# Kernel tuning notes

Measured on AMD Instinct MI355X. Metric: run time of the kernel, lower is better.

## Reference

```python
import jax, jax.numpy as jnp
import numpy as np

HEAD_SIZE = 64
BLOCK_SIZE = 4096
BATCH = 4


def setup_inputs() -> dict:
    key = jax.random.key(0)
    kx, kk, kq, kv = jax.random.split(key, 4)
    x = jax.random.normal(kx, (BATCH, BLOCK_SIZE, HEAD_SIZE), dtype=jnp.float32)
    s = HEAD_SIZE ** -0.5  # ~ torch default linear init scale
    Wk = jax.random.uniform(kk, (HEAD_SIZE, HEAD_SIZE), jnp.float32, -s, s)
    Wq = jax.random.uniform(kq, (HEAD_SIZE, HEAD_SIZE), jnp.float32, -s, s)
    Wv = jax.random.uniform(kv, (HEAD_SIZE, HEAD_SIZE), jnp.float32, -s, s)
    return {"x": x, "Wk": Wk, "Wq": Wq, "Wv": Wv}


def reference(x, Wk, Wq, Wv):
    # x: [B, T, C]; W*: [C, C] stored torch-style (out, in) -> y = x @ W.T
    B, T, C = x.shape
    k = x @ Wk.T  # [B, T, C]
    q = x @ Wq.T
    v = x @ Wv.T
    scores = jnp.einsum('btc,bsc->bts', q, k) * (C ** -0.5)  # [B, T, T]
    causal = jnp.tril(jnp.ones((T, T), dtype=bool))
    scores = jnp.where(causal, scores, -jnp.inf)
    weights = jax.nn.softmax(scores, axis=-1)
    out = jnp.einsum('bts,bsc->btc', weights, v)  # [B, T, C]
    return out
```

## Files before the change

kernel.cpp:

```cpp
#include <hip/hip_runtime.h>
#include <hip/hip_bf16.h>

typedef unsigned short u16;
typedef unsigned int u32;
typedef __bf16 bf16x8_t __attribute__((ext_vector_type(8)));
typedef float f32x4_t __attribute__((ext_vector_type(4)));

constexpr int Bb = 4;
constexpr int Tt = 4096;
constexpr int Dd = 64;
constexpr float QSCALE = 0.18033688011112042f;

__device__ __forceinline__ u16 f2bf(float f) {
  unsigned int u = __builtin_bit_cast(unsigned int, f);
  return (u16)((u + 0x7fffu + ((u >> 16) & 1u)) >> 16);
}
__device__ __forceinline__ u32 pk2(float a, float b) {
  return (u32)f2bf(a) | ((u32)f2bf(b) << 16);
}
__device__ __forceinline__ u32 pkt(float a, float b) {
  const u32 ua = __builtin_bit_cast(u32, a);
  const u32 ub = __builtin_bit_cast(u32, b);
  return (ua >> 16) | (ub & 0xFFFF0000u);
}
__device__ __forceinline__ bf16x8_t ld16(const u16* p) {
  int4 v = *(const int4*)p;
  return __builtin_bit_cast(bf16x8_t, v);
}
__device__ __forceinline__ f32x4_t mfma16(bf16x8_t a, bf16x8_t b, f32x4_t c) {
  return __builtin_amdgcn_mfma_f32_16x16x32_bf16(a, b, c, 0, 0, 0);
}

__global__ __launch_bounds__(256) void HeadV1_proj(
    const float* __restrict__ x, const float* __restrict__ Wk,
    const float* __restrict__ Wq, const float* __restrict__ Wv,
    u16* __restrict__ qS, u16* __restrict__ kS, u16* __restrict__ vS)
{
  __shared__ u16 xl[64][72];
  __shared__ u16 Wl[3][64][72];
  __shared__ u16 ylds[64][72];

  const int t = threadIdx.x;
  const int w = t >> 6, lane = t & 63, l15 = lane & 15, quad = lane >> 4;
  const int r0 = blockIdx.x * 64;
  const int b  = r0 >> 12;
  const int kt = (r0 & 4095) >> 6;
  const long tilebase = ((long)(b * 64 + kt)) * 4096;

  {
    const float* srcs[4] = {x + (long)r0 * 64, Wk, Wq, Wv};
    u16* dstl[4] = {&xl[0][0], &Wl[0][0][0], &Wl[1][0][0], &Wl[2][0][0]};
    #pragma unroll
    for (int mm = 0; mm < 4; mm++) {
      const float* s = srcs[mm];
      u16* d = dstl[mm];
      #pragma unroll
      for (int i = 0; i < 4; i++) {
        const int f4 = i * 256 + t;
        const int row = f4 >> 4, c4 = f4 & 15;
        float4 v = ((const float4*)(s + row * 64))[c4];
        uint2 pk;
        pk.x = pk2(v.x, v.y);
        pk.y = pk2(v.z, v.w);
        *(uint2*)(d + row * 72 + c4 * 4) = pk;
      }
    }
  }
  __syncthreads();

  bf16x8_t xf[2];
  #pragma unroll
  for (int kh = 0; kh < 2; kh++)
    xf[kh] = ld16(&xl[w * 16 + l15][kh * 32 + quad * 8]);

  u16* dsts[3];
  dsts[0] = kS + tilebase; dsts[1] = qS + tilebase; dsts[2] = vS + tilebase;

  #pragma unroll
  for (int m = 0; m < 3; m++) {
    float vals[4][4];
    #pragma unroll
    for (int g = 0; g < 4; g++) {
      f32x4_t acc = {0.f, 0.f, 0.f, 0.f};
      #pragma unroll
      for (int kh = 0; kh < 2; kh++) {
        bf16x8_t wf = ld16(&Wl[m][g * 16 + l15][kh * 32 + quad * 8]);
        acc = mfma16(xf[kh], wf, acc);
      }
      #pragma unroll
      for (int r = 0; r < 4; r++)
        vals[g][r] = (m == 1) ? acc[r] * QSCALE : acc[r];
    }
    #pragma unroll
    for (int g = 0; g < 4; g++)
      #pragma unroll
      for (int r = 0; r < 4; r++)
        ylds[w * 16 + quad * 4 + r][g * 16 + l15] = f2bf(vals[g][r]);
    __syncthreads();
    if (m < 2) {
      #pragma unroll
      for (int kk = 0; kk < 2; kk++) {
        bf16x8_t f = ld16(&ylds[w * 16 + l15][kk * 32 + quad * 8]);
        *(int4*)(dsts[m] + (w * 2 + kk) * 512 + lane * 8) = __builtin_bit_cast(int4, f);
      }
    } else {
      #pragma unroll
      for (int kk = 0; kk < 2; kk++) {
        u16 tmp[8];
        #pragma unroll
        for (int j = 0; j < 8; j++)
          tmp[j] = ylds[kk * 32 + quad * 8 + j][w * 16 + l15];
        *(int4*)(dsts[2] + (kk * 4 + w) * 512 + lane * 8) = *(const int4*)tmp;
      }
    }
    __syncthreads();
  }
}

__global__ __launch_bounds__(1024, 4) void HeadV1_flash(
    const u16* __restrict__ qS, const u16* __restrict__ kS,
    const u16* __restrict__ vS, float* __restrict__ outg)
{
  __shared__ __align__(16) char smem[53248];
  u16  (*pT)[32][36]   = (u16 (*)[32][36])smem;
  float (*chk)[16][33] = (float (*)[16][33])smem;
  float (*stg)[32][68] = (float (*)[32][68])(smem + 33792);
  float (*lst)[32]     = (float (*)[32])(smem + 33792 + 17408);

  const int t    = threadIdx.x;
  const int w    = t >> 6;
  const int lane = t & 63;
  const int l15  = lane & 15;
  const int quad = lane >> 4;

  const int b  = blockIdx.x & 3;
  const int i  = blockIdx.x >> 2;
  const int j1 = i, j2 = 127 - i;
  const int nk1 = (j1 >> 1) + 1;
  const int nk2 = (j2 >> 1) + 1;
  int n1 = (16 * nk1 + 32) / 65;
  if (n1 < 1) n1 = 1;
  if (n1 > 15) n1 = 15;

  const bool grp2 = (w >= n1);
  const int j   = grp2 ? j2 : j1;
  const int nk  = grp2 ? nk2 : nk1;
  const int str = grp2 ? (16 - n1) : n1;
  const int off = grp2 ? (w - n1) : w;

  const int qt64 = j >> 1;
  const int ql0  = (j & 1) * 32;
  const int qr0  = j * 32;
  const long base = (long)b * Tt * Dd;

  union { u32 u4[4]; bf16x8_t v; } uo;
  uo.u4[0] = uo.u4[1] = uo.u4[2] = uo.u4[3] = 0x3F803F80u;
  const bf16x8_t ones = uo.v;
  const f32x4_t zero4 = {0.f, 0.f, 0.f, 0.f};

  const u16* qtile = qS + ((long)(b * 64 + qt64)) * 4096 + lane * 8;
  bf16x8_t qfrag[2][2];
  #pragma unroll
  for (int ct = 0; ct < 2; ct++)
    #pragma unroll
    for (int kd = 0; kd < 2; kd++)
      qfrag[ct][kd] = ld16(qtile + ((ql0 / 16 + ct) * 2 + kd) * 512);

  f32x4_t O[4][2];
  #pragma unroll
  for (int a = 0; a < 4; a++)
    #pragma unroll
    for (int c = 0; c < 2; c++)
      O[a][c] = zero4;
  f32x4_t Lc[2] = {zero4, zero4};

  for (int kt = off; kt < nk; kt += str) {
    const bool ismask = (kt == nk - 1);
    const int kv0 = kt * 64;
    const u16* ktile = kS + ((long)(b * 64 + kt)) * 4096 + lane * 8;
    const u16* vtile = vS + ((long)(b * 64 + kt)) * 4096 + lane * 8;

    #pragma unroll
    for (int kk = 0; kk < 2; kk++) {
      bf16x8_t vf[4];
      #pragma unroll
      for (int dt = 0; dt < 4; dt++)
        vf[dt] = ld16(vtile + (kk * 4 + dt) * 512);

      #pragma unroll
      for (int rtl = 0; rtl < 2; rtl++) {
        const int rt = kk * 2 + rtl;
        bf16x8_t kf0 = ld16(ktile + (rt * 2 + 0) * 512);
        bf16x8_t kf1 = ld16(ktile + (rt * 2 + 1) * 512);
        #pragma unroll
        for (int ct = 0; ct < 2; ct++) {
          f32x4_t acc = zero4;
          acc = mfma16(kf0, qfrag[ct][0], acc);
          acc = mfma16(kf1, qfrag[ct][1], acc);
          if (ismask) {
            const int kvl = kv0 + rt * 16 + quad * 4;
            const int qi  = qr0 + ct * 16 + l15;
            #pragma unroll
            for (int r = 0; r < 4; r++)
              if (kvl + r > qi) acc[r] = -1e30f;
          }
          const float p0 = __builtin_amdgcn_exp2f(acc[0]);
          const float p1 = __builtin_amdgcn_exp2f(acc[1]);
          const float p2 = __builtin_amdgcn_exp2f(acc[2]);
          const float p3 = __builtin_amdgcn_exp2f(acc[3]);
          uint2 pk;
          pk.x = pkt(p0, p1);
          pk.y = pkt(p2, p3);
          *(uint2*)&pT[w][ct * 16 + l15][rtl * 16 + quad * 4] = pk;
        }
      }
      #pragma unroll
      for (int ct = 0; ct < 2; ct++) {
        bf16x8_t pf = ld16(&pT[w][ct * 16 + l15][quad * 8]);
        #pragma unroll
        for (int dt = 0; dt < 4; dt++)
          O[dt][ct] = mfma16(vf[dt], pf, O[dt][ct]);
        Lc[ct] = mfma16(ones, pf, Lc[ct]);
      }
    }
  }

  if (quad == 0) {
    #pragma unroll
    for (int ct = 0; ct < 2; ct++)
      lst[w][ct * 16 + l15] = Lc[ct][0];
  }
  __syncthreads();

  #pragma unroll
  for (int dt = 0; dt < 4; dt++) {
    #pragma unroll
    for (int ct = 0; ct < 2; ct++)
      #pragma unroll
      for (int r = 0; r < 4; r++)
        chk[w][quad * 4 + r][ct * 16 + l15] = O[dt][ct][r];
    __syncthreads();
    {
      const int jsel = t >> 9, tt = t & 511;
      const int d2 = tt >> 5, q = tt & 31;
      const int lo = jsel ? n1 : 0, hi = jsel ? 16 : n1;
      float s = 0.f;
      for (int w2 = lo; w2 < hi; w2++) s += chk[w2][d2][q];
      stg[jsel][q][dt * 16 + d2] = s;
    }
    __syncthreads();
  }

  {
    const int jsel = t >> 9, tt = t & 511;
    const int q = tt >> 4, dg = tt & 15;
    const int lo = jsel ? n1 : 0, hi = jsel ? 16 : n1;
    float L = 0.f;
    for (int w2 = lo; w2 < hi; w2++) L += lst[w2][q];
    const float invL = 1.0f / L;
    const int jj = jsel ? j2 : j1;
    float4 v = *(const float4*)&stg[jsel][q][dg * 4];
    v.x *= invL; v.y *= invL; v.z *= invL; v.w *= invL;
    *(float4*)(outg + base + (long)(jj * 32 + q) * 64 + dg * 4) = v;
  }
}

extern "C" void kernel_launch(void* const* d_in, const int* in_sizes, int n_in,
                              void* d_out, int out_size, void* d_ws, size_t ws_size,
                              hipStream_t stream) {
  (void)in_sizes; (void)n_in; (void)out_size; (void)ws_size;
  const float* x  = (const float*)d_in[0];
  const float* Wk = (const float*)d_in[1];
  const float* Wq = (const float*)d_in[2];
  const float* Wv = (const float*)d_in[3];
  float* out = (float*)d_out;
  u16* qw  = (u16*)d_ws;
  u16* kw  = qw + (size_t)Bb * Tt * Dd;
  u16* vw  = kw + (size_t)Bb * Tt * Dd;

  HeadV1_proj<<<(Bb * Tt) / 64, 256, 0, stream>>>(x, Wk, Wq, Wv, qw, kw, vw);
  HeadV1_flash<<<256, 1024, 0, stream>>>(qw, kw, vw, out);
}
```

Baseline: 84.59 us.

## Software-pipeline QK and PV stages with double-buffered P and scalar row sums

Splits the inner flash loop into an A stage (QK^T, mask, exp, pack to LDS) and a B stage (PV MFMAs), double-buffers the per-wave P tile so stage B of one half-tile overlaps stage A of the next, and prefetches the next K/V fragments a phase ahead. The row-sum MFMA against a ones vector is replaced by scalar accumulation of the truncated bf16 probabilities, which are reduced per quad in LDS at the end. It also raises the priority of the PV MFMA block. LDS use grows to 80 KB per block, which could limit occupancy, and the register pressure from prefetching grows.

```diff
diff --git a/kernel.cpp b/kernel.cpp
--- a/kernel.cpp
+++ b/kernel.cpp
@@ -17,11 +17,6 @@
 }
 __device__ __forceinline__ u32 pk2(float a, float b) {
   return (u32)f2bf(a) | ((u32)f2bf(b) << 16);
-}
-__device__ __forceinline__ u32 pkt(float a, float b) {
-  const u32 ua = __builtin_bit_cast(u32, a);
-  const u32 ub = __builtin_bit_cast(u32, b);
-  return (ua >> 16) | (ub & 0xFFFF0000u);
 }
 __device__ __forceinline__ bf16x8_t ld16(const u16* p) {
   int4 v = *(const int4*)p;
@@ -121,11 +116,11 @@
     const u16* __restrict__ qS, const u16* __restrict__ kS,
     const u16* __restrict__ vS, float* __restrict__ outg)
 {
-  __shared__ __align__(16) char smem[53248];
-  u16  (*pT)[32][36]   = (u16 (*)[32][36])smem;
-  float (*chk)[16][33] = (float (*)[16][33])smem;
-  float (*stg)[32][68] = (float (*)[32][68])(smem + 33792);
-  float (*lst)[32]     = (float (*)[32])(smem + 33792 + 17408);
+  __shared__ __align__(16) char smem[81920];
+  u16  (*pT)[2][32][36] = (u16 (*)[2][32][36])smem;
+  float (*chk)[16][33]  = (float (*)[16][33])smem;
+  float (*stg)[32][68]  = (float (*)[32][68])(smem + 33792);
+  float (*lst)[4][32]   = (float (*)[4][32])(smem + 73728);
 
   const int t    = threadIdx.x;
   const int w    = t >> 6;
@@ -153,9 +148,6 @@
   const int qr0  = j * 32;
   const long base = (long)b * Tt * Dd;
 
-  union { u32 u4[4]; bf16x8_t v; } uo;
-  uo.u4[0] = uo.u4[1] = uo.u4[2] = uo.u4[3] = 0x3F803F80u;
-  const bf16x8_t ones = uo.v;
   const f32x4_t zero4 = {0.f, 0.f, 0.f, 0.f};
 
   const u16* qtile = qS + ((long)(b * 64 + qt64)) * 4096 + lane * 8;
@@ -172,64 +164,95 @@
     #pragma unroll
     for (int c = 0; c < 2; c++)
       O[a][c] = zero4;
-  f32x4_t Lc[2] = {zero4, zero4};
-
-  for (int kt = off; kt < nk; kt += str) {
-    const bool ismask = (kt == nk - 1);
-    const int kv0 = kt * 64;
-    const u16* ktile = kS + ((long)(b * 64 + kt)) * 4096 + lane * 8;
-    const u16* vtile = vS + ((long)(b * 64 + kt)) * 4096 + lane * 8;
-
-    #pragma unroll
-    for (int kk = 0; kk < 2; kk++) {
-      bf16x8_t vf[4];
-      #pragma unroll
-      for (int dt = 0; dt < 4; dt++)
-        vf[dt] = ld16(vtile + (kk * 4 + dt) * 512);
-
-      #pragma unroll
-      for (int rtl = 0; rtl < 2; rtl++) {
-        const int rt = kk * 2 + rtl;
-        bf16x8_t kf0 = ld16(ktile + (rt * 2 + 0) * 512);
-        bf16x8_t kf1 = ld16(ktile + (rt * 2 + 1) * 512);
-        #pragma unroll
-        for (int ct = 0; ct < 2; ct++) {
-          f32x4_t acc = zero4;
-          acc = mfma16(kf0, qfrag[ct][0], acc);
-          acc = mfma16(kf1, qfrag[ct][1], acc);
-          if (ismask) {
-            const int kvl = kv0 + rt * 16 + quad * 4;
-            const int qi  = qr0 + ct * 16 + l15;
-            #pragma unroll
-            for (int r = 0; r < 4; r++)
-              if (kvl + r > qi) acc[r] = -1e30f;
-          }
-          const float p0 = __builtin_amdgcn_exp2f(acc[0]);
-          const float p1 = __builtin_amdgcn_exp2f(acc[1]);
-          const float p2 = __builtin_amdgcn_exp2f(acc[2]);
-          const float p3 = __builtin_amdgcn_exp2f(acc[3]);
-          uint2 pk;
-          pk.x = pkt(p0, p1);
-          pk.y = pkt(p2, p3);
-          *(uint2*)&pT[w][ct * 16 + l15][rtl * 16 + quad * 4] = pk;
+  float Lp[2] = {0.f, 0.f};
+
+  const u16* kb = kS + ((long)(b * 64)) * 4096 + lane * 8;
+  const u16* vb = vS + ((long)(b * 64)) * 4096 + lane * 8;
+
+  auto Astage = [&](int kt_, int kk_, int par_, const bf16x8_t* kf) {
+    const bool ismask = (kt_ == nk - 1);
+    const int kv0 = kt_ * 64;
+    #pragma unroll
+    for (int rtl = 0; rtl < 2; rtl++) {
+      const int rt = kk_ * 2 + rtl;
+      #pragma unroll
+      for (int ct = 0; ct < 2; ct++) {
+        f32x4_t acc = zero4;
+        acc = mfma16(kf[2 * rtl + 0], qfrag[ct][0], acc);
+        acc = mfma16(kf[2 * rtl + 1], qfrag[ct][1], acc);
+        if (ismask) {
+          const int kvl = kv0 + rt * 16 + quad * 4;
+          const int qi  = qr0 + ct * 16 + l15;
+          #pragma unroll
+          for (int r = 0; r < 4; r++)
+            if (kvl + r > qi) acc[r] = -1e30f;
         }
-      }
-      #pragma unroll
-      for (int ct = 0; ct < 2; ct++) {
-        bf16x8_t pf = ld16(&pT[w][ct * 16 + l15][quad * 8]);
-        #pragma unroll
-        for (int dt = 0; dt < 4; dt++)
-          O[dt][ct] = mfma16(vf[dt], pf, O[dt][ct]);
-        Lc[ct] = mfma16(ones, pf, Lc[ct]);
-      }
-    }
-  }
-
-  if (quad == 0) {
-    #pragma unroll
-    for (int ct = 0; ct < 2; ct++)
-      lst[w][ct * 16 + l15] = Lc[ct][0];
-  }
+        const float p0 = __builtin_amdgcn_exp2f(acc[0]);
+        const float p1 = __builtin_amdgcn_exp2f(acc[1]);
+        const float p2 = __builtin_amdgcn_exp2f(acc[2]);
+        const float p3 = __builtin_amdgcn_exp2f(acc[3]);
+        const u32 u0 = __builtin_bit_cast(u32, p0);
+        const u32 u1 = __builtin_bit_cast(u32, p1);
+        const u32 u2 = __builtin_bit_cast(u32, p2);
+        const u32 u3 = __builtin_bit_cast(u32, p3);
+        const u32 h1 = u1 & 0xFFFF0000u, h3 = u3 & 0xFFFF0000u;
+        const float q0 = __builtin_bit_cast(float, u0 & 0xFFFF0000u);
+        const float q1 = __builtin_bit_cast(float, h1);
+        const float q2 = __builtin_bit_cast(float, u2 & 0xFFFF0000u);
+        const float q3 = __builtin_bit_cast(float, h3);
+        Lp[ct] += (q0 + q1) + (q2 + q3);
+        uint2 pk;
+        pk.x = (u0 >> 16) | h1;
+        pk.y = (u2 >> 16) | h3;
+        *(uint2*)&pT[w][par_][ct * 16 + l15][rtl * 16 + quad * 4] = pk;
+      }
+    }
+  };
+
+  auto Bstage = [&](int par_, const bf16x8_t* vf) {
+    bf16x8_t pf0 = ld16(&pT[w][par_][l15][quad * 8]);
+    bf16x8_t pf1 = ld16(&pT[w][par_][16 + l15][quad * 8]);
+    __builtin_amdgcn_s_setprio(1);
+    #pragma unroll
+    for (int dt = 0; dt < 4; dt++) {
+      O[dt][0] = mfma16(vf[dt], pf0, O[dt][0]);
+      O[dt][1] = mfma16(vf[dt], pf1, O[dt][1]);
+    }
+    __builtin_amdgcn_s_setprio(0);
+  };
+
+  const int nv  = (nk - 1 - off) / str + 1;
+  const int nph = 2 * nv;
+
+  bf16x8_t vfC[4];
+  {
+    const u16* kt_ = kb + (long)off * 4096;
+    const u16* vt_ = vb + (long)off * 4096;
+    bf16x8_t kfT[4];
+    #pragma unroll
+    for (int f = 0; f < 4; f++) { kfT[f] = ld16(kt_ + f * 512); vfC[f] = ld16(vt_ + f * 512); }
+    Astage(off, 0, 0, kfT);
+  }
+  int par = 0;
+
+  for (int ph = 1; ph < nph; ph++) {
+    const int ktP = off + (ph >> 1) * str;
+    const int kkP = ph & 1;
+    const u16* kt_ = kb + (long)ktP * 4096 + kkP * 2048;
+    const u16* vt_ = vb + (long)ktP * 4096 + kkP * 2048;
+    bf16x8_t kfT[4], vfN[4];
+    #pragma unroll
+    for (int f = 0; f < 4; f++) { kfT[f] = ld16(kt_ + f * 512); vfN[f] = ld16(vt_ + f * 512); }
+    Bstage(par, vfC);
+    Astage(ktP, kkP, par ^ 1, kfT);
+    #pragma unroll
+    for (int f = 0; f < 4; f++) vfC[f] = vfN[f];
+    par ^= 1;
+  }
+  Bstage(par, vfC);
+
+  lst[w][quad][l15]      = Lp[0];
+  lst[w][quad][16 + l15] = Lp[1];
   __syncthreads();
 
   #pragma unroll
@@ -256,7 +279,10 @@
     const int q = tt >> 4, dg = tt & 15;
     const int lo = jsel ? n1 : 0, hi = jsel ? 16 : n1;
     float L = 0.f;
-    for (int w2 = lo; w2 < hi; w2++) L += lst[w2][q];
+    for (int w2 = lo; w2 < hi; w2++) {
+      #pragma unroll
+      for (int qd = 0; qd < 4; qd++) L += lst[w2][qd][q];
+    }
     const float invL = 1.0f / L;
     const int jj = jsel ? j2 : j1;
     float4 v = *(const float4*)&stg[jsel][q][dg * 4];
```

Measured after the change: 85.89 us. No clear change (+1.5%).

## Fuse projection and flash attention into one cooperative kernel with grid sync

Applied to the files above, without the earlier changes.

Merges the QKV projection kernel and the flash-attention kernel into one cooperative launch of 256 blocks of 1024 threads. Each block projects one 64-row tile, with 12 of its 16 waves computing K, Q and V in parallel, then a grid-wide sync precedes the attention phase. This removes one kernel launch and the inter-kernel gap. In exchange it adds a grid barrier, a cooperative launch, and a larger shared-memory footprint, and it drops the restrict qualifiers on the workspace pointers.

```diff
diff --git a/kernel.cpp b/kernel.cpp
--- a/kernel.cpp
+++ b/kernel.cpp
@@ -1,5 +1,8 @@
 #include <hip/hip_runtime.h>
 #include <hip/hip_bf16.h>
+#include <hip/hip_cooperative_groups.h>
+
+namespace cg = cooperative_groups;
 
 typedef unsigned short u16;
 typedef unsigned int u32;
@@ -31,101 +34,12 @@
   return __builtin_amdgcn_mfma_f32_16x16x32_bf16(a, b, c, 0, 0, 0);
 }
 
-__global__ __launch_bounds__(256) void HeadV1_proj(
+__global__ __launch_bounds__(1024, 4) void HeadV1_fused(
     const float* __restrict__ x, const float* __restrict__ Wk,
     const float* __restrict__ Wq, const float* __restrict__ Wv,
-    u16* __restrict__ qS, u16* __restrict__ kS, u16* __restrict__ vS)
+    u16* qS, u16* kS, u16* vS, float* outg)
 {
-  __shared__ u16 xl[64][72];
-  __shared__ u16 Wl[3][64][72];
-  __shared__ u16 ylds[64][72];
-
-  const int t = threadIdx.x;
-  const int w = t >> 6, lane = t & 63, l15 = lane & 15, quad = lane >> 4;
-  const int r0 = blockIdx.x * 64;
-  const int b  = r0 >> 12;
-  const int kt = (r0 & 4095) >> 6;
-  const long tilebase = ((long)(b * 64 + kt)) * 4096;
-
-  {
-    const float* srcs[4] = {x + (long)r0 * 64, Wk, Wq, Wv};
-    u16* dstl[4] = {&xl[0][0], &Wl[0][0][0], &Wl[1][0][0], &Wl[2][0][0]};
-    #pragma unroll
-    for (int mm = 0; mm < 4; mm++) {
-      const float* s = srcs[mm];
-      u16* d = dstl[mm];
-      #pragma unroll
-      for (int i = 0; i < 4; i++) {
-        const int f4 = i * 256 + t;
-        const int row = f4 >> 4, c4 = f4 & 15;
-        float4 v = ((const float4*)(s + row * 64))[c4];
-        uint2 pk;
-        pk.x = pk2(v.x, v.y);
-        pk.y = pk2(v.z, v.w);
-        *(uint2*)(d + row * 72 + c4 * 4) = pk;
-      }
-    }
-  }
-  __syncthreads();
-
-  bf16x8_t xf[2];
-  #pragma unroll
-  for (int kh = 0; kh < 2; kh++)
-    xf[kh] = ld16(&xl[w * 16 + l15][kh * 32 + quad * 8]);
-
-  u16* dsts[3];
-  dsts[0] = kS + tilebase; dsts[1] = qS + tilebase; dsts[2] = vS + tilebase;
-
-  #pragma unroll
-  for (int m = 0; m < 3; m++) {
-    float vals[4][4];
-    #pragma unroll
-    for (int g = 0; g < 4; g++) {
-      f32x4_t acc = {0.f, 0.f, 0.f, 0.f};
-      #pragma unroll
-      for (int kh = 0; kh < 2; kh++) {
-        bf16x8_t wf = ld16(&Wl[m][g * 16 + l15][kh * 32 + quad * 8]);
-        acc = mfma16(xf[kh], wf, acc);
-      }
-      #pragma unroll
-      for (int r = 0; r < 4; r++)
-        vals[g][r] = (m == 1) ? acc[r] * QSCALE : acc[r];
-    }
-    #pragma unroll
-    for (int g = 0; g < 4; g++)
-      #pragma unroll
-      for (int r = 0; r < 4; r++)
-        ylds[w * 16 + quad * 4 + r][g * 16 + l15] = f2bf(vals[g][r]);
-    __syncthreads();
-    if (m < 2) {
-      #pragma unroll
-      for (int kk = 0; kk < 2; kk++) {
-        bf16x8_t f = ld16(&ylds[w * 16 + l15][kk * 32 + quad * 8]);
-        *(int4*)(dsts[m] + (w * 2 + kk) * 512 + lane * 8) = __builtin_bit_cast(int4, f);
-      }
-    } else {
-      #pragma unroll
-      for (int kk = 0; kk < 2; kk++) {
-        u16 tmp[8];
-        #pragma unroll
-        for (int j = 0; j < 8; j++)
-          tmp[j] = ylds[kk * 32 + quad * 8 + j][w * 16 + l15];
-        *(int4*)(dsts[2] + (kk * 4 + w) * 512 + lane * 8) = *(const int4*)tmp;
-      }
-    }
-    __syncthreads();
-  }
-}
-
-__global__ __launch_bounds__(1024, 4) void HeadV1_flash(
-    const u16* __restrict__ qS, const u16* __restrict__ kS,
-    const u16* __restrict__ vS, float* __restrict__ outg)
-{
-  __shared__ __align__(16) char smem[53248];
-  u16  (*pT)[32][36]   = (u16 (*)[32][36])smem;
-  float (*chk)[16][33] = (float (*)[16][33])smem;
-  float (*stg)[32][68] = (float (*)[32][68])(smem + 33792);
-  float (*lst)[32]     = (float (*)[32])(smem + 33792 + 17408);
+  __shared__ __align__(16) char smem[65536];
 
   const int t    = threadIdx.x;
   const int w    = t >> 6;
@@ -133,135 +47,223 @@
   const int l15  = lane & 15;
   const int quad = lane >> 4;
 
-  const int b  = blockIdx.x & 3;
-  const int i  = blockIdx.x >> 2;
-  const int j1 = i, j2 = 127 - i;
-  const int nk1 = (j1 >> 1) + 1;
-  const int nk2 = (j2 >> 1) + 1;
-  int n1 = (16 * nk1 + 32) / 65;
-  if (n1 < 1) n1 = 1;
-  if (n1 > 15) n1 = 15;
-
-  const bool grp2 = (w >= n1);
-  const int j   = grp2 ? j2 : j1;
-  const int nk  = grp2 ? nk2 : nk1;
-  const int str = grp2 ? (16 - n1) : n1;
-  const int off = grp2 ? (w - n1) : w;
-
-  const int qt64 = j >> 1;
-  const int ql0  = (j & 1) * 32;
-  const int qr0  = j * 32;
-  const long base = (long)b * Tt * Dd;
-
-  union { u32 u4[4]; bf16x8_t v; } uo;
-  uo.u4[0] = uo.u4[1] = uo.u4[2] = uo.u4[3] = 0x3F803F80u;
-  const bf16x8_t ones = uo.v;
-  const f32x4_t zero4 = {0.f, 0.f, 0.f, 0.f};
-
-  const u16* qtile = qS + ((long)(b * 64 + qt64)) * 4096 + lane * 8;
-  bf16x8_t qfrag[2][2];
-  #pragma unroll
-  for (int ct = 0; ct < 2; ct++)
-    #pragma unroll
-    for (int kd = 0; kd < 2; kd++)
-      qfrag[ct][kd] = ld16(qtile + ((ql0 / 16 + ct) * 2 + kd) * 512);
-
-  f32x4_t O[4][2];
-  #pragma unroll
-  for (int a = 0; a < 4; a++)
-    #pragma unroll
-    for (int c = 0; c < 2; c++)
-      O[a][c] = zero4;
-  f32x4_t Lc[2] = {zero4, zero4};
-
-  for (int kt = off; kt < nk; kt += str) {
-    const bool ismask = (kt == nk - 1);
-    const int kv0 = kt * 64;
-    const u16* ktile = kS + ((long)(b * 64 + kt)) * 4096 + lane * 8;
-    const u16* vtile = vS + ((long)(b * 64 + kt)) * 4096 + lane * 8;
-
-    #pragma unroll
-    for (int kk = 0; kk < 2; kk++) {
-      bf16x8_t vf[4];
-      #pragma unroll
-      for (int dt = 0; dt < 4; dt++)
-        vf[dt] = ld16(vtile + (kk * 4 + dt) * 512);
-
-      #pragma unroll
-      for (int rtl = 0; rtl < 2; rtl++) {
-        const int rt = kk * 2 + rtl;
-        bf16x8_t kf0 = ld16(ktile + (rt * 2 + 0) * 512);
-        bf16x8_t kf1 = ld16(ktile + (rt * 2 + 1) * 512);
-        #pragma unroll
-        for (int ct = 0; ct < 2; ct++) {
-          f32x4_t acc = zero4;
-          acc = mfma16(kf0, qfrag[ct][0], acc);
-          acc = mfma16(kf1, qfrag[ct][1], acc);
-          if (ismask) {
-            const int kvl = kv0 + rt * 16 + quad * 4;
-            const int qi  = qr0 + ct * 16 + l15;
-            #pragma unroll
-            for (int r = 0; r < 4; r++)
-              if (kvl + r > qi) acc[r] = -1e30f;
-          }
-          const float p0 = __builtin_amdgcn_exp2f(acc[0]);
-          const float p1 = __builtin_amdgcn_exp2f(acc[1]);
-          const float p2 = __builtin_amdgcn_exp2f(acc[2]);
-          const float p3 = __builtin_amdgcn_exp2f(acc[3]);
-          uint2 pk;
-          pk.x = pkt(p0, p1);
-          pk.y = pkt(p2, p3);
-          *(uint2*)&pT[w][ct * 16 + l15][rtl * 16 + quad * 4] = pk;
-        }
-      }
-      #pragma unroll
-      for (int ct = 0; ct < 2; ct++) {
-        bf16x8_t pf = ld16(&pT[w][ct * 16 + l15][quad * 8]);
-        #pragma unroll
-        for (int dt = 0; dt < 4; dt++)
-          O[dt][ct] = mfma16(vf[dt], pf, O[dt][ct]);
-        Lc[ct] = mfma16(ones, pf, Lc[ct]);
+  {
+    u16 (*xl)[72]    = (u16 (*)[72])smem;
+    u16 (*Wl)[64][72] = (u16 (*)[64][72])(smem + 9216);
+    u16 (*yl)[64][72] = (u16 (*)[64][72])(smem + 36864);
+
+    const int blk = blockIdx.x;
+    const int r0 = blk * 64;
+    const int b  = blk >> 6;
+    const int kt = blk & 63;
+    const long tilebase = ((long)(b * 64 + kt)) * 4096;
+
+    {
+      const float* srcs[4] = {x + (long)r0 * 64, Wk, Wq, Wv};
+      u16* dstl[4] = {&xl[0][0], &Wl[0][0][0], &Wl[1][0][0], &Wl[2][0][0]};
+      const int row = t >> 4, c4 = t & 15;
+      #pragma unroll
+      for (int mm = 0; mm < 4; mm++) {
+        float4 v = ((const float4*)(srcs[mm] + row * 64))[c4];
+        uint2 pk;
+        pk.x = pk2(v.x, v.y);
+        pk.y = pk2(v.z, v.w);
+        *(uint2*)(dstl[mm] + row * 72 + c4 * 4) = pk;
+      }
+    }
+    __syncthreads();
+
+    const int mg = w >> 2;
+    const int wl = w & 3;
+    if (mg < 3) {
+      bf16x8_t xf[2];
+      #pragma unroll
+      for (int kh = 0; kh < 2; kh++)
+        xf[kh] = ld16(&xl[wl * 16 + l15][kh * 32 + quad * 8]);
+
+      float vals[4][4];
+      #pragma unroll
+      for (int g = 0; g < 4; g++) {
+        f32x4_t acc = {0.f, 0.f, 0.f, 0.f};
+        #pragma unroll
+        for (int kh = 0; kh < 2; kh++) {
+          bf16x8_t wf = ld16(&Wl[mg][g * 16 + l15][kh * 32 + quad * 8]);
+          acc = mfma16(xf[kh], wf, acc);
+        }
+        #pragma unroll
+        for (int r = 0; r < 4; r++)
+          vals[g][r] = (mg == 1) ? acc[r] * QSCALE : acc[r];
+      }
+      #pragma unroll
+      for (int g = 0; g < 4; g++)
+        #pragma unroll
+        for (int r = 0; r < 4; r++)
+          yl[mg][wl * 16 + quad * 4 + r][g * 16 + l15] = f2bf(vals[g][r]);
+    }
+    __syncthreads();
+
+    if (mg < 3) {
+      u16* dsts[3];
+      dsts[0] = kS + tilebase; dsts[1] = qS + tilebase; dsts[2] = vS + tilebase;
+      if (mg < 2) {
+        #pragma unroll
+        for (int kk = 0; kk < 2; kk++) {
+          bf16x8_t f = ld16(&yl[mg][wl * 16 + l15][kk * 32 + quad * 8]);
+          *(int4*)(dsts[mg] + (wl * 2 + kk) * 512 + lane * 8) = __builtin_bit_cast(int4, f);
+        }
+      } else {
+        #pragma unroll
+        for (int kk = 0; kk < 2; kk++) {
+          u16 tmp[8];
+          #pragma unroll
+          for (int jj = 0; jj < 8; jj++)
+            tmp[jj] = yl[2][kk * 32 + quad * 8 + jj][wl * 16 + l15];
+          *(int4*)(dsts[2] + (kk * 4 + wl) * 512 + lane * 8) = *(const int4*)tmp;
+        }
       }
     }
   }
 
-  if (quad == 0) {
+  cg::this_grid().sync();
+
+  {
+    u16  (*pT)[2 * 36 * 32]= (u16 (*)[2*36*32])smem;
+    u16  (*pT2)[32][36]   = (u16 (*)[32][36])smem;
+    float (*chk)[16][33]  = (float (*)[16][33])smem;
+    float (*stg)[32][68]  = (float (*)[32][68])(smem + 33792);
+    float (*lst)[32]      = (float (*)[32])(smem + 51200);
+    (void)pT;
+
+    const int b  = blockIdx.x & 3;
+    const int i  = blockIdx.x >> 2;
+    const int j1 = i, j2 = 127 - i;
+    const int nk1 = (j1 >> 1) + 1;
+    const int nk2 = (j2 >> 1) + 1;
+    int n1 = (16 * nk1 + 32) / 65;
+    if (n1 < 1) n1 = 1;
+    if (n1 > 15) n1 = 15;
+
+    const bool grp2 = (w >= n1);
+    const int j   = grp2 ? j2 : j1;
+    const int nk  = grp2 ? nk2 : nk1;
+    const int str = grp2 ? (16 - n1) : n1;
+    const int off = grp2 ? (w - n1) : w;
+
+    const int qt64 = j >> 1;
+    const int ql0  = (j & 1) * 32;
+    const int qr0  = j * 32;
+    const long base = (long)b * Tt * Dd;
+
+    union { u32 u4[4]; bf16x8_t v; } uo;
+    uo.u4[0] = uo.u4[1] = uo.u4[2] = uo.u4[3] = 0x3F803F80u;
+    const bf16x8_t ones = uo.v;
+    const f32x4_t zero4 = {0.f, 0.f, 0.f, 0.f};
+
+    const u16* qtile = qS + ((long)(b * 64 + qt64)) * 4096 + lane * 8;
+    bf16x8_t qfrag[2][2];
     #pragma unroll
     for (int ct = 0; ct < 2; ct++)
-      lst[w][ct * 16 + l15] = Lc[ct][0];
-  }
-  __syncthreads();
-
-  #pragma unroll
-  for (int dt = 0; dt < 4; dt++) {
+      #pragma unroll
+      for (int kd = 0; kd < 2; kd++)
+        qfrag[ct][kd] = ld16(qtile + ((ql0 / 16 + ct) * 2 + kd) * 512);
+
+    f32x4_t O[4][2];
     #pragma unroll
-    for (int ct = 0; ct < 2; ct++)
-      #pragma unroll
-      for (int r = 0; r < 4; r++)
-        chk[w][quad * 4 + r][ct * 16 + l15] = O[dt][ct][r];
+    for (int a = 0; a < 4; a++)
+      #pragma unroll
+      for (int c = 0; c < 2; c++)
+        O[a][c] = zero4;
+    f32x4_t Lc[2] = {zero4, zero4};
+
+    for (int kt = off; kt < nk; kt += str) {
+      const bool ismask = (kt == nk - 1);
+      const int kv0 = kt * 64;
+      const u16* ktile = kS + ((long)(b * 64 + kt)) * 4096 + lane * 8;
+      const u16* vtile = vS + ((long)(b * 64 + kt)) * 4096 + lane * 8;
+
+      #pragma unroll
+      for (int kk = 0; kk < 2; kk++) {
+        bf16x8_t vf[4];
+        #pragma unroll
+        for (int dt = 0; dt < 4; dt++)
+          vf[dt] = ld16(vtile + (kk * 4 + dt) * 512);
+
+        #pragma unroll
+        for (int rtl = 0; rtl < 2; rtl++) {
+          const int rt = kk * 2 + rtl;
+          bf16x8_t kf0 = ld16(ktile + (rt * 2 + 0) * 512);
+          bf16x8_t kf1 = ld16(ktile + (rt * 2 + 1) * 512);
+          #pragma unroll
+          for (int ct = 0; ct < 2; ct++) {
+            f32x4_t acc = zero4;
+            acc = mfma16(kf0, qfrag[ct][0], acc);
+            acc = mfma16(kf1, qfrag[ct][1], acc);
+            if (ismask) {
+              const int kvl = kv0 + rt * 16 + quad * 4;
+              const int qi  = qr0 + ct * 16 + l15;
+              #pragma unroll
+              for (int r = 0; r < 4; r++)
+                if (kvl + r > qi) acc[r] = -1e30f;
+            }
+            const float p0 = __builtin_amdgcn_exp2f(acc[0]);
+            const float p1 = __builtin_amdgcn_exp2f(acc[1]);
+            const float p2 = __builtin_amdgcn_exp2f(acc[2]);
+            const float p3 = __builtin_amdgcn_exp2f(acc[3]);
+            uint2 pk;
+            pk.x = pkt(p0, p1);
+            pk.y = pkt(p2, p3);
+            *(uint2*)&pT2[w][ct * 16 + l15][rtl * 16 + quad * 4] = pk;
+          }
+        }
+        #pragma unroll
+        for (int ct = 0; ct < 2; ct++) {
+          bf16x8_t pf = ld16(&pT2[w][ct * 16 + l15][quad * 8]);
+          #pragma unroll
+          for (int dt = 0; dt < 4; dt++)
+            O[dt][ct] = mfma16(vf[dt], pf, O[dt][ct]);
+          Lc[ct] = mfma16(ones, pf, Lc[ct]);
+        }
+      }
+    }
+
+    if (quad == 0) {
+      #pragma unroll
+      for (int ct = 0; ct < 2; ct++)
+        lst[w][ct * 16 + l15] = Lc[ct][0];
+    }
     __syncthreads();
+
+    #pragma unroll
+    for (int dt = 0; dt < 4; dt++) {
+      #pragma unroll
+      for (int ct = 0; ct < 2; ct++)
+        #pragma unroll
+        for (int r = 0; r < 4; r++)
+          chk[w][quad * 4 + r][ct * 16 + l15] = O[dt][ct][r];
+      __syncthreads();
+      {
+        const int jsel = t >> 9, tt = t & 511;
+        const int d2 = tt >> 5, q = tt & 31;
+        const int lo = jsel ? n1 : 0, hi = jsel ? 16 : n1;
+        float s = 0.f;
+        for (int w2 = lo; w2 < hi; w2++) s += chk[w2][d2][q];
+        stg[jsel][q][dt * 16 + d2] = s;
+      }
+      __syncthreads();
+    }
+
     {
       const int jsel = t >> 9, tt = t & 511;
-      const int d2 = tt >> 5, q = tt & 31;
+      const int q = tt >> 4, dg = tt & 15;
       const int lo = jsel ? n1 : 0, hi = jsel ? 16 : n1;
-      float s = 0.f;
-      for (int w2 = lo; w2 < hi; w2++) s += chk[w2][d2][q];
-      stg[jsel][q][dt * 16 + d2] = s;
-    }
-    __syncthreads();
-  }
-
-  {
-    const int jsel = t >> 9, tt = t & 511;
-    const int q = tt >> 4, dg = tt & 15;
-    const int lo = jsel ? n1 : 0, hi = jsel ? 16 : n1;
-    float L = 0.f;
-    for (int w2 = lo; w2 < hi; w2++) L += lst[w2][q];
-    const float invL = 1.0f / L;
-    const int jj = jsel ? j2 : j1;
-    float4 v = *(const float4*)&stg[jsel][q][dg * 4];
-    v.x *= invL; v.y *= invL; v.z *= invL; v.w *= invL;
-    *(float4*)(outg + base + (long)(jj * 32 + q) * 64 + dg * 4) = v;
+      float L = 0.f;
+      for (int w2 = lo; w2 < hi; w2++) L += lst[w2][q];
+      const float invL = 1.0f / L;
+      const int jj = jsel ? j2 : j1;
+      float4 v = *(const float4*)&stg[jsel][q][dg * 4];
+      v.x *= invL; v.y *= invL; v.z *= invL; v.w *= invL;
+      *(float4*)(outg + base + (long)(jj * 32 + q) * 64 + dg * 4) = v;
+    }
   }
 }
 
@@ -278,6 +280,8 @@
   u16* kw  = qw + (size_t)Bb * Tt * Dd;
   u16* vw  = kw + (size_t)Bb * Tt * Dd;
 
-  HeadV1_proj<<<(Bb * Tt) / 64, 256, 0, stream>>>(x, Wk, Wq, Wv, qw, kw, vw);
-  HeadV1_flash<<<256, 1024, 0, stream>>>(qw, kw, vw, out);
-}
+  void* kargs[] = {(void*)&x, (void*)&Wk, (void*)&Wq, (void*)&Wv,
+                   (void*)&qw, (void*)&kw, (void*)&vw, (void*)&out};
+  hipLaunchCooperativeKernel((void*)HeadV1_fused, dim3(256), dim3(1024),
+                             kargs, 0, stream);
+}
```

Measured after the change: 130.7 us. +54.5%, slower.
